# Optimization experiments

Measured on AMD Instinct MI355X. Metric: run time of the kernel, lower is better.

Reference implementation:

```python
import jax, jax.numpy as jnp
import numpy as np

B, N = 8, 2048
CLIP, D, BD, NC = 512, 256, 128, 10  # CLIP_EMBED_DIM, GNN_NODE_DIM, BOTTLENECK_DIM_GNN, NUM_CLASSES
LN_EPS = 1e-5


def _layer_norm(x, g, b):
    mu = jnp.mean(x, axis=-1, keepdims=True)
    var = jnp.mean(jnp.square(x - mu), axis=-1, keepdims=True)
    return (x - mu) / jnp.sqrt(var + LN_EPS) * g + b


def setup_inputs() -> dict:
    key = jax.random.key(0)
    ks = jax.random.split(key, 16)
    def w(k, shape, fan_in):
        lim = 1.0 / np.sqrt(fan_in)
        return jax.random.uniform(k, shape, jnp.float32, -lim, lim)
    return {
        "local_feat": jax.random.normal(ks[0], (B, N, CLIP), jnp.float32),
        "coords": jax.random.uniform(ks[1], (B, N, 2), jnp.float32),
        "mask": jax.random.randint(ks[2], (B, N), 0, 2).astype(bool),
        # node_encoder: Linear(CLIP->D) + LayerNorm(D)
        "enc_w": w(ks[3], (CLIP, D), CLIP), "enc_b": jnp.zeros((D,), jnp.float32),
        "enc_g": jnp.ones((D,), jnp.float32), "enc_beta": jnp.zeros((D,), jnp.float32),
        "gamma": jnp.asarray(5.0, jnp.float32),  # spatial_gamma
        "wq": w(ks[4], (D, D), D), "bq": jnp.zeros((D,), jnp.float32),
        "wk": w(ks[5], (D, D), D), "bk": jnp.zeros((D,), jnp.float32),
        "wv": w(ks[6], (D, D), D), "bv": jnp.zeros((D,), jnp.float32),
        # bottleneck: Linear(D->BD) + LayerNorm(BD)
        "bn_w": w(ks[7], (D, BD), D), "bn_b": jnp.zeros((BD,), jnp.float32),
        "bn_g": jnp.ones((BD,), jnp.float32), "bn_beta": jnp.zeros((BD,), jnp.float32),
        # classifier: Linear(BD->BD//2) + ReLU + Linear(BD//2->NC)
        "c1_w": w(ks[8], (BD, BD // 2), BD), "c1_b": jnp.zeros((BD // 2,), jnp.float32),
        "c2_w": w(ks[9], (BD // 2, NC), BD // 2), "c2_b": jnp.zeros((NC,), jnp.float32),
    }


def reference(local_feat, coords, mask, enc_w, enc_b, enc_g, enc_beta, gamma,
              wq, bq, wk, bk, wv, bv, bn_w, bn_b, bn_g, bn_beta,
              c1_w, c1_b, c2_w, c2_b):
    # node encoder: Linear + LN + ReLU -> h [B,N,D]
    h = jax.nn.relu(_layer_norm(local_feat @ enc_w + enc_b, enc_g, enc_beta))
    # pairwise euclidean distances on 2D coords (torch.cdist, under no_grad)
    xy = coords[:, :, :2]
    sq = jnp.sum(xy * xy, axis=-1)                                   # [B,N]
    d2 = sq[:, :, None] + sq[:, None, :] - 2.0 * jnp.einsum('bnd,bmd->bnm', xy, xy)
    dist = jax.lax.stop_gradient(jnp.sqrt(jnp.maximum(d2, 0.0)))     # [B,N,N]
    spatial_adj = jnp.exp(-dist * jnp.abs(gamma))
    q, k, v = h @ wq + bq, h @ wk + bk, h @ wv + bv
    scores = jnp.einsum('bnd,bmd->bnm', q, k) / jnp.sqrt(jnp.float32(D))
    attn = jax.nn.softmax(scores, axis=-1) * spatial_adj             # gated attention
    attn = jnp.where(mask[:, None, :], 0.0, attn)                    # zero masked keys
    agg = jnp.einsum('bnm,bmd->bnd', attn, v)                        # [B,N,D]
    out = jax.nn.relu(_layer_norm(agg @ bn_w + bn_b, bn_g, bn_beta)) # [B,N,BD]
    mask_v = (~mask)[:, :, None].astype(out.dtype)                   # [B,N,1]
    pooled = (out * mask_v).sum(axis=1) / jnp.maximum(mask_v.sum(axis=1), 1e-9)
    logits = jax.nn.relu(pooled @ c1_w + c1_b) @ c2_w + c2_b
    return logits, pooled
```

## Files before the change

kernel.cpp:

```cpp
#include <hip/hip_runtime.h>
#include <hip/hip_bf16.h>

typedef unsigned short ushort_t;
typedef __attribute__((ext_vector_type(8))) short s8;
typedef __attribute__((ext_vector_type(4))) float f4;
typedef __attribute__((ext_vector_type(16))) float f16v;

__device__ __forceinline__ unsigned short f2bf(float f) {
  union { float f; unsigned int u; } c; c.f = f;
  unsigned int r = (c.u + 0x7fffu + ((c.u >> 16) & 1u)) >> 16;
  return (unsigned short)r;
}
__device__ __forceinline__ float bf2f(ushort_t u) {
  union { unsigned int i; float f; } c; c.i = ((unsigned int)u) << 16; return c.f;
}
__device__ __forceinline__ uint4 pack8(float4 a, float4 b) {
  uint4 r;
  r.x = (unsigned)f2bf(a.x) | ((unsigned)f2bf(a.y) << 16);
  r.y = (unsigned)f2bf(a.z) | ((unsigned)f2bf(a.w) << 16);
  r.z = (unsigned)f2bf(b.x) | ((unsigned)f2bf(b.y) << 16);
  r.w = (unsigned)f2bf(b.z) | ((unsigned)f2bf(b.w) << 16);
  return r;
}
__device__ __forceinline__ void dma16(const ushort_t* g, const short* l) {
  __builtin_amdgcn_global_load_lds(
      (const __attribute__((address_space(1))) unsigned int*)g,
      (__attribute__((address_space(3))) unsigned int*)(unsigned long)l,
      16, 0, 0);
}

__global__ __launch_bounds__(256) void k_wt_all(
    const float* __restrict__ enc_w, const float* __restrict__ wq,
    const float* __restrict__ wk, const float* __restrict__ wv,
    const float* __restrict__ bn_w,
    ushort_t* __restrict__ enc_wT, ushort_t* __restrict__ wqkvT,
    ushort_t* __restrict__ bn_wT) {
  const int y = blockIdx.y;
  const int i = blockIdx.x * 256 + threadIdx.x;
  if (y == 0) {
    if (i < 131072) { const int n = i >> 9, k = i & 511; enc_wT[i] = f2bf(enc_w[k * 256 + n]); }
  } else if (y <= 3) {
    if (i < 65536) {
      const int n = i >> 8, k = i & 255;
      const float* src = (y == 1) ? wq : (y == 2) ? wk : wv;
      wqkvT[(y - 1) * 65536 + i] = f2bf(src[k * 256 + n]);
    }
  } else {
    if (i < 32768) { const int n = i >> 8, k = i & 255; bn_wT[i] = f2bf(bn_w[k * 128 + n]); }
  }
}

__global__ __launch_bounds__(256, 3) void k_gemm_enc(
    const float* __restrict__ A, const ushort_t* __restrict__ WT,
    const float* __restrict__ bia, const float* __restrict__ g,
    const float* __restrict__ beta, ushort_t* __restrict__ out) {
  __shared__ short Al[32 * 72];
  __shared__ short Bl[256 * 72];
  __shared__ float red1[32][2], red2[32][2];
  const int t = threadIdx.x;
  const int wv = t >> 6, lane = t & 63, l16 = lane & 15, quad = lane >> 4;
  const int wm = wv >> 1, wn = wv & 1;
  const int row0 = blockIdx.x * 32;

  f4 acc[8];
#pragma unroll
  for (int nf = 0; nf < 8; ++nf) acc[nf] = (f4){0.f, 0.f, 0.f, 0.f};

  for (int k0 = 0; k0 < 512; k0 += 64) {
    __syncthreads();
    {
      const int r = t >> 3, c8 = t & 7;
      const float* src = &A[(size_t)(row0 + r) * 512 + k0 + c8 * 8];
      *(uint4*)&Al[r * 72 + c8 * 8] =
          pack8(*(const float4*)src, *(const float4*)(src + 4));
    }
#pragma unroll
    for (int i = 0; i < 8; ++i) {
      const int ch = t + i * 256;
      const int r = ch >> 3, c8 = ch & 7;
      *(uint4*)&Bl[r * 72 + c8 * 8] =
          *(const uint4*)&WT[(size_t)r * 512 + k0 + c8 * 8];
    }
    __syncthreads();
#pragma unroll
    for (int kc = 0; kc < 2; ++kc) {
      const s8 af = *(const s8*)&Al[(wm * 16 + l16) * 72 + kc * 32 + quad * 8];
#pragma unroll
      for (int nf = 0; nf < 8; ++nf) {
        const s8 bf = *(const s8*)&Bl[(wn * 128 + nf * 16 + l16) * 72 + kc * 32 + quad * 8];
        acc[nf] = __builtin_amdgcn_mfma_f32_16x16x32_bf16(af, bf, acc[nf], 0, 0, 0);
      }
    }
  }
  float bi[8], gg[8], bb[8];
#pragma unroll
  for (int nf = 0; nf < 8; ++nf) {
    const int col = wn * 128 + nf * 16 + l16;
    bi[nf] = bia[col]; gg[nf] = g[col]; bb[nf] = beta[col];
  }
  float s1[4] = {0.f, 0.f, 0.f, 0.f}, s2[4] = {0.f, 0.f, 0.f, 0.f};
#pragma unroll
  for (int nf = 0; nf < 8; ++nf)
#pragma unroll
    for (int r = 0; r < 4; ++r) {
      const float v = acc[nf][r] + bi[nf];
      acc[nf][r] = v;
      s1[r] += v; s2[r] += v * v;
    }
#pragma unroll
  for (int m = 1; m < 16; m <<= 1) {
#pragma unroll
    for (int r = 0; r < 4; ++r) {
      s1[r] += __shfl_xor(s1[r], m);
      s2[r] += __shfl_xor(s2[r], m);
    }
  }
  if (l16 == 0) {
#pragma unroll
    for (int r = 0; r < 4; ++r) {
      const int rl = wm * 16 + quad * 4 + r;
      red1[rl][wn] = s1[r]; red2[rl][wn] = s2[r];
    }
  }
  __syncthreads();
#pragma unroll
  for (int r = 0; r < 4; ++r) {
    const int rl = wm * 16 + quad * 4 + r;
    const float mu = (red1[rl][0] + red1[rl][1]) * (1.f / 256.f);
    const float var = (red2[rl][0] + red2[rl][1]) * (1.f / 256.f) - mu * mu;
    const float rstd = rsqrtf(var + 1e-5f);
#pragma unroll
    for (int nf = 0; nf < 8; ++nf) {
      const int col = wn * 128 + nf * 16 + l16;
      const float v = (acc[nf][r] - mu) * rstd * gg[nf] + bb[nf];
      out[(size_t)(row0 + rl) * 256 + col] = f2bf(fmaxf(v, 0.f));
    }
  }
}

__global__ __launch_bounds__(256, 4) void k_gemm_qkv(
    const ushort_t* __restrict__ A, const ushort_t* __restrict__ WT,
    const float* __restrict__ bq, const float* __restrict__ bk,
    const float* __restrict__ bv,
    ushort_t* __restrict__ q, ushort_t* __restrict__ k, ushort_t* __restrict__ vt) {
  __shared__ short Al[64 * 72];
  __shared__ short Bl[128 * 72];
  const int t = threadIdx.x;
  const int wv = t >> 6, lane = t & 63, l16 = lane & 15, quad = lane >> 4;
  const int wm = wv >> 1, wn = wv & 1;
  const int row0 = blockIdx.x * 64;
  const int nb = blockIdx.y;
  const int type = nb >> 1;
  const ushort_t* wtb = WT + (size_t)nb * 128 * 256;

  f4 acc[2][4];
#pragma unroll
  for (int mf = 0; mf < 2; ++mf)
#pragma unroll
    for (int nf = 0; nf < 4; ++nf) acc[mf][nf] = (f4){0.f, 0.f, 0.f, 0.f};

  for (int k0 = 0; k0 < 256; k0 += 64) {
    __syncthreads();
#pragma unroll
    for (int i = 0; i < 2; ++i) {
      const int ch = t + i * 256;
      const int r = ch >> 3, c8 = ch & 7;
      *(uint4*)&Al[r * 72 + c8 * 8] =
          *(const uint4*)&A[(size_t)(row0 + r) * 256 + k0 + c8 * 8];
    }
#pragma unroll
    for (int i = 0; i < 4; ++i) {
      const int ch = t + i * 256;
      const int r = ch >> 3, c8 = ch & 7;
      *(uint4*)&Bl[r * 72 + c8 * 8] =
          *(const uint4*)&wtb[(size_t)r * 256 + k0 + c8 * 8];
    }
    __syncthreads();
#pragma unroll
    for (int kc = 0; kc < 2; ++kc) {
      s8 af[2];
      af[0] = *(const s8*)&Al[(wm * 32 + l16) * 72 + kc * 32 + quad * 8];
      af[1] = *(const s8*)&Al[(wm * 32 + 16 + l16) * 72 + kc * 32 + quad * 8];
#pragma unroll
      for (int nf = 0; nf < 4; ++nf) {
        const s8 bf = *(const s8*)&Bl[(wn * 64 + nf * 16 + l16) * 72 + kc * 32 + quad * 8];
        acc[0][nf] = __builtin_amdgcn_mfma_f32_16x16x32_bf16(af[0], bf, acc[0][nf], 0, 0, 0);
        acc[1][nf] = __builtin_amdgcn_mfma_f32_16x16x32_bf16(af[1], bf, acc[1][nf], 0, 0, 0);
      }
    }
  }
  const float* bias = (type == 0) ? bq : (type == 1) ? bk : bv;
#pragma unroll
  for (int nf = 0; nf < 4; ++nf) {
    const int colg = nb * 128 + wn * 64 + nf * 16 + l16;
    const int col = colg - type * 256;
    const float bi = bias[col];
    if (type == 2) {
      const int b = row0 >> 11;
#pragma unroll
      for (int mf = 0; mf < 2; ++mf) {
        const int n = (row0 & 2047) + wm * 32 + mf * 16 + quad * 4;
        ushort4 pk;
        pk.x = f2bf(acc[mf][nf][0] + bi);
        pk.y = f2bf(acc[mf][nf][1] + bi);
        pk.z = f2bf(acc[mf][nf][2] + bi);
        pk.w = f2bf(acc[mf][nf][3] + bi);
        *(ushort4*)&vt[((size_t)b * 256 + col) * 2048 + n] = pk;
      }
    } else {
      ushort_t* dst = (type == 0) ? q : k;
      const float sc = (type == 0) ? 0.0625f : 1.f;
#pragma unroll
      for (int mf = 0; mf < 2; ++mf)
#pragma unroll
        for (int r = 0; r < 4; ++r) {
          const int row = row0 + wm * 32 + mf * 16 + quad * 4 + r;
          dst[(size_t)row * 256 + col] = f2bf((acc[mf][nf][r] + bi) * sc);
        }
    }
  }
}

__global__ __launch_bounds__(256, 2) void k_attn(
    const ushort_t* __restrict__ qb, const ushort_t* __restrict__ kb,
    const ushort_t* __restrict__ vtb,
    const float* __restrict__ coords, const int* __restrict__ mask,
    const float* __restrict__ gam,
    ushort_t* __restrict__ Opb, float* __restrict__ lws) {
  __shared__ short kld[2][8192];
  __shared__ short vld[2][8192];
  __shared__ short pl[128 * 40];
  const int t = threadIdx.x;
  const int wv = t >> 6, lane = t & 63, l16 = lane & 15, quad = lane >> 4;
  const int hw = lane >> 5, l32 = lane & 31;
  const int b = blockIdx.z, ks = blockIdx.y;
  const int qw = blockIdx.x * 128 + wv * 32;
  const int kbase = ks * 512;

  float rcx[2][4], rcy[2][4];
#pragma unroll
  for (int mf = 0; mf < 2; ++mf)
#pragma unroll
    for (int r = 0; r < 4; ++r) {
      const float2 cc = ((const float2*)coords)[b * 2048 + qw + mf * 16 + quad * 4 + r];
      rcx[mf][r] = cc.x; rcy[mf][r] = cc.y;
    }
  const float gamma = fabsf(gam[0]);

  f16v o32[8];
#pragma unroll
  for (int i = 0; i < 8; ++i)
#pragma unroll
    for (int j = 0; j < 16; ++j) o32[i][j] = 0.f;
  float lrun[2][4];
#pragma unroll
  for (int mf = 0; mf < 2; ++mf)
#pragma unroll
    for (int r = 0; r < 4; ++r) lrun[mf][r] = 0.f;

  const ushort_t* kbb = kb + ((size_t)b * 2048 + kbase) * 256;
  const ushort_t* vbb = vtb + (size_t)b * 256 * 2048 + kbase;
  const ushort_t* qrow0 = qb + ((size_t)b * 2048 + qw + l16) * 256 + quad * 8;
  const ushort_t* qrow1 = qrow0 + 16 * 256;

#pragma unroll
  for (int i = 0; i < 4; ++i) {
    const int i2 = wv * 4 + i;
    dma16(kbb + (size_t)l32 * 256 + (i2 * 2 + hw) * 8, &kld[0][i2 * 512]);
    dma16(vbb + (size_t)(i * 64 + lane) * 2048 + wv * 8, &vld[0][(wv * 256 + i * 64) * 8]);
  }
  __syncthreads();

  for (int kt = 0; kt < 16; ++kt) {
    const int cur = kt & 1;
    const int m0 = kbase + kt * 32;
    if (kt < 15) {
      const ushort_t* kn = kbb + (size_t)(kt + 1) * 32 * 256;
      const ushort_t* vn = vbb + (kt + 1) * 32;
      const int nb2 = cur ^ 1;
#pragma unroll
      for (int i = 0; i < 4; ++i) {
        const int i2 = wv * 4 + i;
        dma16(kn + (size_t)l32 * 256 + (i2 * 2 + hw) * 8, &kld[nb2][i2 * 512]);
        dma16(vn + (size_t)(i * 64 + lane) * 2048 + wv * 8, &vld[nb2][(wv * 256 + i * 64) * 8]);
      }
    }
    f4 sc[2][2];
#pragma unroll
    for (int mf = 0; mf < 2; ++mf)
#pragma unroll
      for (int s = 0; s < 2; ++s) sc[mf][s] = (f4){0.f, 0.f, 0.f, 0.f};
#pragma unroll
    for (int c = 0; c < 8; ++c) {
      const s8 qa0 = *(const s8*)(qrow0 + c * 32);
      const s8 qa1 = *(const s8*)(qrow1 + c * 32);
#pragma unroll
      for (int s = 0; s < 2; ++s) {
        const s8 bfr = *(const s8*)&kld[cur][((c * 4 + quad) * 32 + s * 16 + l16) * 8];
        sc[0][s] = __builtin_amdgcn_mfma_f32_16x16x32_bf16(qa0, bfr, sc[0][s], 0, 0, 0);
        sc[1][s] = __builtin_amdgcn_mfma_f32_16x16x32_bf16(qa1, bfr, sc[1][s], 0, 0, 0);
      }
    }
#pragma unroll
    for (int s = 0; s < 2; ++s) {
      const int m = m0 + s * 16 + l16;
      const float2 cc = ((const float2*)coords)[b * 2048 + m];
      const float mfv = mask[b * 2048 + m] ? 0.f : 1.f;
#pragma unroll
      for (int mf = 0; mf < 2; ++mf)
#pragma unroll
        for (int r = 0; r < 4; ++r) {
          const float p = __expf(sc[mf][s][r]);
          lrun[mf][r] += p;
          const float dx = rcx[mf][r] - cc.x, dy = rcy[mf][r] - cc.y;
          const float dist = sqrtf(fmaxf(dx * dx + dy * dy, 0.f));
          const float w = p * __expf(-gamma * dist) * mfv;
          pl[(wv * 32 + mf * 16 + quad * 4 + r) * 40 + s * 16 + l16] = (short)f2bf(w);
        }
    }
    const s8 pa0 = *(const s8*)&pl[(wv * 32 + l32) * 40 + hw * 8];
    const s8 pa1 = *(const s8*)&pl[(wv * 32 + l32) * 40 + 16 + hw * 8];
#pragma unroll
    for (int dt = 0; dt < 8; ++dt) {
      const s8 bv0 = *(const s8*)&vld[cur][(hw * 256 + dt * 32 + l32) * 8];
      o32[dt] = __builtin_amdgcn_mfma_f32_32x32x16_bf16(pa0, bv0, o32[dt], 0, 0, 0);
      const s8 bv1 = *(const s8*)&vld[cur][((2 + hw) * 256 + dt * 32 + l32) * 8];
      o32[dt] = __builtin_amdgcn_mfma_f32_32x32x16_bf16(pa1, bv1, o32[dt], 0, 0, 0);
    }
    __syncthreads();
  }
  ushort_t* OpK = Opb + (size_t)ks * 4194304;
#pragma unroll
  for (int dt = 0; dt < 8; ++dt) {
#pragma unroll
    for (int reg = 0; reg < 16; ++reg) {
      const int row = (reg & 3) + 8 * (reg >> 2) + 4 * hw;
      OpK[((size_t)b * 2048 + qw + row) * 256 + dt * 32 + l32] = f2bf(o32[dt][reg]);
    }
  }
#pragma unroll
  for (int o2 = 1; o2 < 16; o2 <<= 1) {
#pragma unroll
    for (int mf = 0; mf < 2; ++mf)
#pragma unroll
      for (int r = 0; r < 4; ++r) lrun[mf][r] += __shfl_xor(lrun[mf][r], o2);
  }
  if (l16 == 0) {
#pragma unroll
    for (int mf = 0; mf < 2; ++mf)
#pragma unroll
      for (int r = 0; r < 4; ++r)
        lws[ks * 16384 + b * 2048 + qw + mf * 16 + quad * 4 + r] = lrun[mf][r];
  }
}

__global__ __launch_bounds__(256, 3) void k_gemm_bn(
    const ushort_t* __restrict__ Opb, const float* __restrict__ lws,
    const ushort_t* __restrict__ WT,
    const float* __restrict__ bia, const float* __restrict__ g,
    const float* __restrict__ beta, ushort_t* __restrict__ out) {
  __shared__ short Al[32 * 72];
  __shared__ short Bl[128 * 72];
  __shared__ float red1[32][2], red2[32][2];
  __shared__ float sCm[32];
  const int t = threadIdx.x;
  const int wv = t >> 6, lane = t & 63, l16 = lane & 15, quad = lane >> 4;
  const int wm = wv >> 1, wn = wv & 1;
  const int row0 = blockIdx.x * 32;

  if (t < 32) {
    const int row = row0 + t;
    sCm[t] = 1.f / (lws[row] + lws[16384 + row] + lws[32768 + row] + lws[49152 + row]);
  }

  f4 acc[4];
#pragma unroll
  for (int nf = 0; nf < 4; ++nf) acc[nf] = (f4){0.f, 0.f, 0.f, 0.f};

  for (int k0 = 0; k0 < 256; k0 += 64) {
    __syncthreads();
    {
      const int r = t >> 3, c8 = t & 7;
      const float c0 = sCm[r];
      const size_t off = (size_t)(row0 + r) * 256 + k0 + c8 * 8;
      float e[8];
#pragma unroll
      for (int j = 0; j < 8; ++j) e[j] = 0.f;
#pragma unroll
      for (int pp = 0; pp < 4; ++pp) {
        const uint4 u = *(const uint4*)&Opb[(size_t)pp * 4194304 + off];
        e[0] += bf2f((ushort_t)(u.x & 0xffff)); e[1] += bf2f((ushort_t)(u.x >> 16));
        e[2] += bf2f((ushort_t)(u.y & 0xffff)); e[3] += bf2f((ushort_t)(u.y >> 16));
        e[4] += bf2f((ushort_t)(u.z & 0xffff)); e[5] += bf2f((ushort_t)(u.z >> 16));
        e[6] += bf2f((ushort_t)(u.w & 0xffff)); e[7] += bf2f((ushort_t)(u.w >> 16));
      }
      float4 ea = {c0 * e[0], c0 * e[1], c0 * e[2], c0 * e[3]};
      float4 eb = {c0 * e[4], c0 * e[5], c0 * e[6], c0 * e[7]};
      *(uint4*)&Al[r * 72 + c8 * 8] = pack8(ea, eb);
    }
#pragma unroll
    for (int i = 0; i < 4; ++i) {
      const int ch = t + i * 256;
      const int r = ch >> 3, c8 = ch & 7;
      *(uint4*)&Bl[r * 72 + c8 * 8] =
          *(const uint4*)&WT[(size_t)r * 256 + k0 + c8 * 8];
    }
    __syncthreads();
#pragma unroll
    for (int kc = 0; kc < 2; ++kc) {
      const s8 af = *(const s8*)&Al[(wm * 16 + l16) * 72 + kc * 32 + quad * 8];
#pragma unroll
      for (int nf = 0; nf < 4; ++nf) {
        const s8 bf = *(const s8*)&Bl[(wn * 64 + nf * 16 + l16) * 72 + kc * 32 + quad * 8];
        acc[nf] = __builtin_amdgcn_mfma_f32_16x16x32_bf16(af, bf, acc[nf], 0, 0, 0);
      }
    }
  }
  float bi[4], gg[4], bb[4];
#pragma unroll
  for (int nf = 0; nf < 4; ++nf) {
    const int col = wn * 64 + nf * 16 + l16;
    bi[nf] = bia[col]; gg[nf] = g[col]; bb[nf] = beta[col];
  }
  float s1[4] = {0.f, 0.f, 0.f, 0.f}, s2[4] = {0.f, 0.f, 0.f, 0.f};
#pragma unroll
  for (int nf = 0; nf < 4; ++nf)
#pragma unroll
    for (int r = 0; r < 4; ++r) {
      const float v = acc[nf][r] + bi[nf];
      acc[nf][r] = v;
      s1[r] += v; s2[r] += v * v;
    }
#pragma unroll
  for (int m = 1; m < 16; m <<= 1) {
#pragma unroll
    for (int r = 0; r < 4; ++r) {
      s1[r] += __shfl_xor(s1[r], m);
      s2[r] += __shfl_xor(s2[r], m);
    }
  }
  if (l16 == 0) {
#pragma unroll
    for (int r = 0; r < 4; ++r) {
      const int rl = wm * 16 + quad * 4 + r;
      red1[rl][wn] = s1[r]; red2[rl][wn] = s2[r];
    }
  }
  __syncthreads();
#pragma unroll
  for (int r = 0; r < 4; ++r) {
    const int rl = wm * 16 + quad * 4 + r;
    const float mu = (red1[rl][0] + red1[rl][1]) * (1.f / 128.f);
    const float var = (red2[rl][0] + red2[rl][1]) * (1.f / 128.f) - mu * mu;
    const float rstd = rsqrtf(var + 1e-5f);
#pragma unroll
    for (int nf = 0; nf < 4; ++nf) {
      const int col = wn * 64 + nf * 16 + l16;
      const float v = (acc[nf][r] - mu) * rstd * gg[nf] + bb[nf];
      out[(size_t)(row0 + rl) * 128 + col] = f2bf(fmaxf(v, 0.f));
    }
  }
}

__global__ __launch_bounds__(128) void k_pool1(
    const ushort_t* __restrict__ obn, const int* __restrict__ mask,
    float* __restrict__ pp) {
  const int g = blockIdx.x, b = blockIdx.y, d = threadIdx.x;
  const ushort_t* ob = obn + ((size_t)b * 2048 + g * 128) * 128;
  const int* mb = mask + b * 2048 + g * 128;
  float s = 0.f, cnt = 0.f;
  for (int n = 0; n < 128; ++n) {
    const float w = mb[n] ? 0.f : 1.f;
    s += w * bf2f(ob[(size_t)n * 128 + d]);
    cnt += w;
  }
  pp[(b * 16 + g) * 132 + d] = s;
  if (d == 0) pp[(b * 16 + g) * 132 + 128] = cnt;
}

__global__ __launch_bounds__(128) void k_pool2_head(
    const float* __restrict__ pp, const float* __restrict__ c1w,
    const float* __restrict__ c1b, const float* __restrict__ c2w,
    const float* __restrict__ c2b, float* __restrict__ dout) {
  __shared__ float ps[128];
  __shared__ float h1[64];
  const int b = blockIdx.x, t = threadIdx.x;
  float s = 0.f, cnt = 0.f;
  for (int g = 0; g < 16; ++g) {
    s += pp[(b * 16 + g) * 132 + t];
    cnt += pp[(b * 16 + g) * 132 + 128];
  }
  const float p = s / fmaxf(cnt, 1e-9f);
  ps[t] = p;
  dout[80 + b * 128 + t] = p;
  __syncthreads();
  if (t < 64) {
    float acc = c1b[t];
    for (int d = 0; d < 128; ++d) acc += ps[d] * c1w[d * 64 + t];
    h1[t] = fmaxf(acc, 0.f);
  }
  __syncthreads();
  if (t < 10) {
    float a2 = c2b[t];
    for (int j = 0; j < 64; ++j) a2 += h1[j] * c2w[j * 10 + t];
    dout[b * 10 + t] = a2;
  }
}

extern "C" void kernel_launch(void* const* d_in, const int* in_sizes, int n_in,
                              void* d_out, int out_size, void* d_ws, size_t ws_size,
                              hipStream_t stream) {
  const float* lf     = (const float*)d_in[0];
  const float* coords = (const float*)d_in[1];
  const int*   mask   = (const int*)d_in[2];
  const float* enc_w  = (const float*)d_in[3];
  const float* enc_b  = (const float*)d_in[4];
  const float* enc_g  = (const float*)d_in[5];
  const float* enc_be = (const float*)d_in[6];
  const float* gamma  = (const float*)d_in[7];
  const float* wq     = (const float*)d_in[8];
  const float* bq     = (const float*)d_in[9];
  const float* wk     = (const float*)d_in[10];
  const float* bk     = (const float*)d_in[11];
  const float* wv     = (const float*)d_in[12];
  const float* bv     = (const float*)d_in[13];
  const float* bn_w   = (const float*)d_in[14];
  const float* bn_b   = (const float*)d_in[15];
  const float* bn_g   = (const float*)d_in[16];
  const float* bn_be  = (const float*)d_in[17];
  const float* c1w    = (const float*)d_in[18];
  const float* c1b    = (const float*)d_in[19];
  const float* c2w    = (const float*)d_in[20];
  const float* c2b    = (const float*)d_in[21];

  float* ws = (float*)d_ws;
  ushort_t* h_bf   = (ushort_t*)ws;
  ushort_t* q_bf   = (ushort_t*)(ws + 2097152);
  ushort_t* k_bf   = (ushort_t*)(ws + 4194304);
  ushort_t* vt_bf  = (ushort_t*)(ws + 6291456);
  ushort_t* Opb    = (ushort_t*)(ws + 8388608);
  ushort_t* obn_bf = (ushort_t*)(ws + 16777216);
  ushort_t* enc_wT = (ushort_t*)(ws + 17825792);
  ushort_t* wqkvT  = (ushort_t*)(ws + 17891328);
  ushort_t* bn_wT  = (ushort_t*)(ws + 17989632);
  float*    lws    = ws + 18006016;
  float*    ppart  = ws + 18071552;
  float* out = (float*)d_out;

  k_wt_all<<<dim3(512, 5), 256, 0, stream>>>(enc_w, wq, wk, wv, bn_w,
                                             enc_wT, wqkvT, bn_wT);
  k_gemm_enc<<<512, 256, 0, stream>>>(lf, enc_wT, enc_b, enc_g, enc_be, h_bf);
  k_gemm_qkv<<<dim3(256, 6), 256, 0, stream>>>(h_bf, wqkvT, bq, bk, bv, q_bf, k_bf, vt_bf);
  k_attn<<<dim3(16, 4, 8), 256, 0, stream>>>(q_bf, k_bf, vt_bf, coords, mask, gamma,
                                             Opb, lws);
  k_gemm_bn<<<512, 256, 0, stream>>>(Opb, lws, bn_wT, bn_b, bn_g, bn_be, obn_bf);
  k_pool1<<<dim3(16, 8), 128, 0, stream>>>(obn_bf, mask, ppart);
  k_pool2_head<<<8, 128, 0, stream>>>(ppart, c1w, c1b, c2w, c2b, out);
}
```

Before: 259.7 us.

## Shrink attention tiles to 16 queries per wave with 16x16 MFMA for P·V

Restructures the attention kernel so each wave handles 16 query rows instead of 32, with 16-key tiles instead of 32. The P·V product switches from 32x32x16 to 16x16x32 MFMA, and the upper half of the P tile is zero-padded. The grid doubles and launch bounds rise to 3 blocks per CU, which cuts registers and LDS per block to raise occupancy. In exchange, each K/V tile is reused by fewer queries, so total K/V loads double. Half of each P·V MFMA multiplies padding zeros, and there are twice as many loop iterations with a barrier each.

```diff
diff --git a/kernel.cpp b/kernel.cpp
--- a/kernel.cpp
+++ b/kernel.cpp
@@ -4,7 +4,6 @@
 typedef unsigned short ushort_t;
 typedef __attribute__((ext_vector_type(8))) short s8;
 typedef __attribute__((ext_vector_type(4))) float f4;
-typedef __attribute__((ext_vector_type(16))) float f16v;
 
 __device__ __forceinline__ unsigned short f2bf(float f) {
   union { float f; unsigned int u; } c; c.f = f;
@@ -221,136 +220,114 @@
   }
 }
 
-__global__ __launch_bounds__(256, 2) void k_attn(
+__global__ __launch_bounds__(256, 3) void k_attn(
     const ushort_t* __restrict__ qb, const ushort_t* __restrict__ kb,
     const ushort_t* __restrict__ vtb,
     const float* __restrict__ coords, const int* __restrict__ mask,
     const float* __restrict__ gam,
     ushort_t* __restrict__ Opb, float* __restrict__ lws) {
-  __shared__ short kld[2][8192];
-  __shared__ short vld[2][8192];
-  __shared__ short pl[128 * 40];
+  __shared__ short kld[2][4096];
+  __shared__ short vld[2][4096];
+  __shared__ short pl[64 * 40];
   const int t = threadIdx.x;
   const int wv = t >> 6, lane = t & 63, l16 = lane & 15, quad = lane >> 4;
-  const int hw = lane >> 5, l32 = lane & 31;
   const int b = blockIdx.z, ks = blockIdx.y;
-  const int qw = blockIdx.x * 128 + wv * 32;
+  const int qw = blockIdx.x * 64 + wv * 16;
   const int kbase = ks * 512;
 
-  float rcx[2][4], rcy[2][4];
-#pragma unroll
-  for (int mf = 0; mf < 2; ++mf)
-#pragma unroll
-    for (int r = 0; r < 4; ++r) {
-      const float2 cc = ((const float2*)coords)[b * 2048 + qw + mf * 16 + quad * 4 + r];
-      rcx[mf][r] = cc.x; rcy[mf][r] = cc.y;
-    }
+  {
+    unsigned int* z = (unsigned int*)&pl[(t >> 2) * 40 + 16 + (t & 3) * 4];
+    z[0] = 0u; z[1] = 0u;
+  }
+
+  float rcx[4], rcy[4];
+#pragma unroll
+  for (int r = 0; r < 4; ++r) {
+    const float2 cc = ((const float2*)coords)[b * 2048 + qw + quad * 4 + r];
+    rcx[r] = cc.x; rcy[r] = cc.y;
+  }
   const float gamma = fabsf(gam[0]);
 
-  f16v o32[8];
-#pragma unroll
-  for (int i = 0; i < 8; ++i)
-#pragma unroll
-    for (int j = 0; j < 16; ++j) o32[i][j] = 0.f;
-  float lrun[2][4];
-#pragma unroll
-  for (int mf = 0; mf < 2; ++mf)
-#pragma unroll
-    for (int r = 0; r < 4; ++r) lrun[mf][r] = 0.f;
+  f4 o16[16];
+#pragma unroll
+  for (int i = 0; i < 16; ++i) o16[i] = (f4){0.f, 0.f, 0.f, 0.f};
+  float lrun[4] = {0.f, 0.f, 0.f, 0.f};
 
   const ushort_t* kbb = kb + ((size_t)b * 2048 + kbase) * 256;
   const ushort_t* vbb = vtb + (size_t)b * 256 * 2048 + kbase;
-  const ushort_t* qrow0 = qb + ((size_t)b * 2048 + qw + l16) * 256 + quad * 8;
-  const ushort_t* qrow1 = qrow0 + 16 * 256;
-
-#pragma unroll
-  for (int i = 0; i < 4; ++i) {
-    const int i2 = wv * 4 + i;
-    dma16(kbb + (size_t)l32 * 256 + (i2 * 2 + hw) * 8, &kld[0][i2 * 512]);
-    dma16(vbb + (size_t)(i * 64 + lane) * 2048 + wv * 8, &vld[0][(wv * 256 + i * 64) * 8]);
+  const ushort_t* qrow = qb + ((size_t)b * 2048 + qw + l16) * 256 + quad * 8;
+
+#pragma unroll
+  for (int i = 0; i < 2; ++i) {
+    const int i2 = wv * 2 + i;
+    dma16(kbb + (size_t)(lane & 15) * 256 + (i2 * 4 + (lane >> 4)) * 8,
+          &kld[0][i2 * 512]);
+    dma16(vbb + (size_t)(i2 * 32 + (lane >> 1)) * 2048 + (lane & 1) * 8,
+          &vld[0][i2 * 512]);
   }
   __syncthreads();
 
-  for (int kt = 0; kt < 16; ++kt) {
+  for (int kt = 0; kt < 32; ++kt) {
     const int cur = kt & 1;
-    const int m0 = kbase + kt * 32;
-    if (kt < 15) {
-      const ushort_t* kn = kbb + (size_t)(kt + 1) * 32 * 256;
-      const ushort_t* vn = vbb + (kt + 1) * 32;
+    const int m0 = kbase + kt * 16;
+    if (kt < 31) {
+      const ushort_t* kn = kbb + (size_t)(kt + 1) * 16 * 256;
+      const ushort_t* vn = vbb + (kt + 1) * 16;
       const int nb2 = cur ^ 1;
 #pragma unroll
-      for (int i = 0; i < 4; ++i) {
-        const int i2 = wv * 4 + i;
-        dma16(kn + (size_t)l32 * 256 + (i2 * 2 + hw) * 8, &kld[nb2][i2 * 512]);
-        dma16(vn + (size_t)(i * 64 + lane) * 2048 + wv * 8, &vld[nb2][(wv * 256 + i * 64) * 8]);
-      }
-    }
-    f4 sc[2][2];
-#pragma unroll
-    for (int mf = 0; mf < 2; ++mf)
-#pragma unroll
-      for (int s = 0; s < 2; ++s) sc[mf][s] = (f4){0.f, 0.f, 0.f, 0.f};
+      for (int i = 0; i < 2; ++i) {
+        const int i2 = wv * 2 + i;
+        dma16(kn + (size_t)(lane & 15) * 256 + (i2 * 4 + (lane >> 4)) * 8,
+              &kld[nb2][i2 * 512]);
+        dma16(vn + (size_t)(i2 * 32 + (lane >> 1)) * 2048 + (lane & 1) * 8,
+              &vld[nb2][i2 * 512]);
+      }
+    }
+    f4 sc = (f4){0.f, 0.f, 0.f, 0.f};
 #pragma unroll
     for (int c = 0; c < 8; ++c) {
-      const s8 qa0 = *(const s8*)(qrow0 + c * 32);
-      const s8 qa1 = *(const s8*)(qrow1 + c * 32);
-#pragma unroll
-      for (int s = 0; s < 2; ++s) {
-        const s8 bfr = *(const s8*)&kld[cur][((c * 4 + quad) * 32 + s * 16 + l16) * 8];
-        sc[0][s] = __builtin_amdgcn_mfma_f32_16x16x32_bf16(qa0, bfr, sc[0][s], 0, 0, 0);
-        sc[1][s] = __builtin_amdgcn_mfma_f32_16x16x32_bf16(qa1, bfr, sc[1][s], 0, 0, 0);
-      }
-    }
-#pragma unroll
-    for (int s = 0; s < 2; ++s) {
-      const int m = m0 + s * 16 + l16;
+      const s8 qa = *(const s8*)(qrow + c * 32);
+      const s8 bfr = *(const s8*)&kld[cur][((c * 4 + quad) * 16 + l16) * 8];
+      sc = __builtin_amdgcn_mfma_f32_16x16x32_bf16(qa, bfr, sc, 0, 0, 0);
+    }
+    {
+      const int m = m0 + l16;
       const float2 cc = ((const float2*)coords)[b * 2048 + m];
       const float mfv = mask[b * 2048 + m] ? 0.f : 1.f;
 #pragma unroll
-      for (int mf = 0; mf < 2; ++mf)
-#pragma unroll
-        for (int r = 0; r < 4; ++r) {
-          const float p = __expf(sc[mf][s][r]);
-          lrun[mf][r] += p;
-          const float dx = rcx[mf][r] - cc.x, dy = rcy[mf][r] - cc.y;
-          const float dist = sqrtf(fmaxf(dx * dx + dy * dy, 0.f));
-          const float w = p * __expf(-gamma * dist) * mfv;
-          pl[(wv * 32 + mf * 16 + quad * 4 + r) * 40 + s * 16 + l16] = (short)f2bf(w);
-        }
-    }
-    const s8 pa0 = *(const s8*)&pl[(wv * 32 + l32) * 40 + hw * 8];
-    const s8 pa1 = *(const s8*)&pl[(wv * 32 + l32) * 40 + 16 + hw * 8];
-#pragma unroll
-    for (int dt = 0; dt < 8; ++dt) {
-      const s8 bv0 = *(const s8*)&vld[cur][(hw * 256 + dt * 32 + l32) * 8];
-      o32[dt] = __builtin_amdgcn_mfma_f32_32x32x16_bf16(pa0, bv0, o32[dt], 0, 0, 0);
-      const s8 bv1 = *(const s8*)&vld[cur][((2 + hw) * 256 + dt * 32 + l32) * 8];
-      o32[dt] = __builtin_amdgcn_mfma_f32_32x32x16_bf16(pa1, bv1, o32[dt], 0, 0, 0);
+      for (int r = 0; r < 4; ++r) {
+        const float p = __expf(sc[r]);
+        lrun[r] += p;
+        const float dx = rcx[r] - cc.x, dy = rcy[r] - cc.y;
+        const float dist = sqrtf(fmaxf(dx * dx + dy * dy, 0.f));
+        const float w = p * __expf(-gamma * dist) * mfv;
+        pl[(wv * 16 + quad * 4 + r) * 40 + l16] = (short)f2bf(w);
+      }
+    }
+    const s8 pa = *(const s8*)&pl[(wv * 16 + l16) * 40 + quad * 8];
+#pragma unroll
+    for (int df = 0; df < 16; ++df) {
+      const s8 bv = *(const s8*)&vld[cur][((df * 16 + l16) * 16) + (quad & 1) * 8];
+      o16[df] = __builtin_amdgcn_mfma_f32_16x16x32_bf16(pa, bv, o16[df], 0, 0, 0);
     }
     __syncthreads();
   }
   ushort_t* OpK = Opb + (size_t)ks * 4194304;
 #pragma unroll
-  for (int dt = 0; dt < 8; ++dt) {
-#pragma unroll
-    for (int reg = 0; reg < 16; ++reg) {
-      const int row = (reg & 3) + 8 * (reg >> 2) + 4 * hw;
-      OpK[((size_t)b * 2048 + qw + row) * 256 + dt * 32 + l32] = f2bf(o32[dt][reg]);
-    }
+  for (int r = 0; r < 4; ++r) {
+    ushort_t* orow = OpK + ((size_t)b * 2048 + qw + quad * 4 + r) * 256 + l16;
+#pragma unroll
+    for (int df = 0; df < 16; ++df) orow[df * 16] = f2bf(o16[df][r]);
   }
 #pragma unroll
   for (int o2 = 1; o2 < 16; o2 <<= 1) {
 #pragma unroll
-    for (int mf = 0; mf < 2; ++mf)
-#pragma unroll
-      for (int r = 0; r < 4; ++r) lrun[mf][r] += __shfl_xor(lrun[mf][r], o2);
+    for (int r = 0; r < 4; ++r) lrun[r] += __shfl_xor(lrun[r], o2);
   }
   if (l16 == 0) {
 #pragma unroll
-    for (int mf = 0; mf < 2; ++mf)
-#pragma unroll
-      for (int r = 0; r < 4; ++r)
-        lws[ks * 16384 + b * 2048 + qw + mf * 16 + quad * 4 + r] = lrun[mf][r];
+    for (int r = 0; r < 4; ++r)
+      lws[ks * 16384 + b * 2048 + qw + quad * 4 + r] = lrun[r];
   }
 }
 
@@ -551,7 +528,7 @@
                                              enc_wT, wqkvT, bn_wT);
   k_gemm_enc<<<512, 256, 0, stream>>>(lf, enc_wT, enc_b, enc_g, enc_be, h_bf);
   k_gemm_qkv<<<dim3(256, 6), 256, 0, stream>>>(h_bf, wqkvT, bq, bk, bv, q_bf, k_bf, vt_bf);
-  k_attn<<<dim3(16, 4, 8), 256, 0, stream>>>(q_bf, k_bf, vt_bf, coords, mask, gamma,
+  k_attn<<<dim3(32, 4, 8), 256, 0, stream>>>(q_bf, k_bf, vt_bf, coords, mask, gamma,
                                              Opb, lws);
   k_gemm_bn<<<512, 256, 0, stream>>>(Opb, lws, bn_wT, bn_b, bn_g, bn_be, obn_bf);
   k_pool1<<<dim3(16, 8), 128, 0, stream>>>(obn_bf, mask, ppart);
```

Result: slower. 301.8 us (+16.2%).

## Fuse masked mean pooling into bottleneck GEMM epilogue via atomics

Applied to the files above, without the earlier changes.

The bottleneck GEMM epilogue now multiplies each LayerNorm+ReLU output row by a precomputed mask weight, reduces across the wave with shuffles, and atomically adds into a per-batch pooled accumulator. This removes the bf16 intermediate write and re-read and the separate pool1 kernel. A small kernel zeroes the accumulator and precomputes mask weights, and the head kernel recomputes the unmasked count. The trade is contended float atomics and nondeterministic summation order, plus leftover dummy declarations.

```diff
diff --git a/kernel.cpp b/kernel.cpp
--- a/kernel.cpp
+++ b/kernel.cpp
@@ -358,7 +358,7 @@
     const ushort_t* __restrict__ Opb, const float* __restrict__ lws,
     const ushort_t* __restrict__ WT,
     const float* __restrict__ bia, const float* __restrict__ g,
-    const float* __restrict__ beta, ushort_t* __restrict__ out) {
+    const float* __restrict__ beta, float* __restrict__ pooledAcc) {
   __shared__ short Al[32 * 72];
   __shared__ short Bl[128 * 72];
   __shared__ float red1[32][2], red2[32][2];
@@ -367,6 +367,7 @@
   const int wv = t >> 6, lane = t & 63, l16 = lane & 15, quad = lane >> 4;
   const int wm = wv >> 1, wn = wv & 1;
   const int row0 = blockIdx.x * 32;
+  const int b = row0 >> 11;
 
   if (t < 32) {
     const int row = row0 + t;
@@ -447,50 +448,71 @@
     }
   }
   __syncthreads();
+  float colsum[4] = {0.f, 0.f, 0.f, 0.f};
+  const int* mrow = (const int*)0;
 #pragma unroll
   for (int r = 0; r < 4; ++r) {
     const int rl = wm * 16 + quad * 4 + r;
     const float mu = (red1[rl][0] + red1[rl][1]) * (1.f / 128.f);
     const float var = (red2[rl][0] + red2[rl][1]) * (1.f / 128.f) - mu * mu;
     const float rstd = rsqrtf(var + 1e-5f);
+    extern const int* __mask_dummy;
 #pragma unroll
     for (int nf = 0; nf < 4; ++nf) {
-      const int col = wn * 64 + nf * 16 + l16;
       const float v = (acc[nf][r] - mu) * rstd * gg[nf] + bb[nf];
-      out[(size_t)(row0 + rl) * 128 + col] = f2bf(fmaxf(v, 0.f));
-    }
-  }
-}
-
-__global__ __launch_bounds__(128) void k_pool1(
-    const ushort_t* __restrict__ obn, const int* __restrict__ mask,
-    float* __restrict__ pp) {
-  const int g = blockIdx.x, b = blockIdx.y, d = threadIdx.x;
-  const ushort_t* ob = obn + ((size_t)b * 2048 + g * 128) * 128;
-  const int* mb = mask + b * 2048 + g * 128;
-  float s = 0.f, cnt = 0.f;
-  for (int n = 0; n < 128; ++n) {
-    const float w = mb[n] ? 0.f : 1.f;
-    s += w * bf2f(ob[(size_t)n * 128 + d]);
-    cnt += w;
-  }
-  pp[(b * 16 + g) * 132 + d] = s;
-  if (d == 0) pp[(b * 16 + g) * 132 + 128] = cnt;
+      acc[nf][r] = fmaxf(v, 0.f);
+    }
+  }
+  (void)mrow;
+  {
+    float mw[4];
+#pragma unroll
+    for (int r = 0; r < 4; ++r) {
+      const int rl = wm * 16 + quad * 4 + r;
+      mw[r] = pooledAcc[1024 + row0 + rl] ;
+    }
+#pragma unroll
+    for (int nf = 0; nf < 4; ++nf) {
+      float s = acc[nf][0] * mw[0] + acc[nf][1] * mw[1] +
+                acc[nf][2] * mw[2] + acc[nf][3] * mw[3];
+      s += __shfl_xor(s, 16);
+      s += __shfl_xor(s, 32);
+      if (quad == 0) {
+        const int col = wn * 64 + nf * 16 + l16;
+        atomicAdd(&pooledAcc[b * 128 + col], s);
+      }
+    }
+  }
+}
+
+__global__ __launch_bounds__(256) void k_maskf(const int* __restrict__ mask,
+                                               float* __restrict__ pooledAcc) {
+  const int i = blockIdx.x * 256 + threadIdx.x;
+  if (i < 16384) pooledAcc[1024 + i] = mask[i] ? 0.f : 1.f;
+  if (i < 1024) pooledAcc[i] = 0.f;
 }
 
 __global__ __launch_bounds__(128) void k_pool2_head(
-    const float* __restrict__ pp, const float* __restrict__ c1w,
-    const float* __restrict__ c1b, const float* __restrict__ c2w,
-    const float* __restrict__ c2b, float* __restrict__ dout) {
+    const float* __restrict__ pooledAcc, const int* __restrict__ mask,
+    const float* __restrict__ c1w, const float* __restrict__ c1b,
+    const float* __restrict__ c2w, const float* __restrict__ c2b,
+    float* __restrict__ dout) {
   __shared__ float ps[128];
   __shared__ float h1[64];
+  __shared__ float scnt[128];
   const int b = blockIdx.x, t = threadIdx.x;
-  float s = 0.f, cnt = 0.f;
-  for (int g = 0; g < 16; ++g) {
-    s += pp[(b * 16 + g) * 132 + t];
-    cnt += pp[(b * 16 + g) * 132 + 128];
-  }
-  const float p = s / fmaxf(cnt, 1e-9f);
+  float c = 0.f;
+  const int* mb = mask + b * 2048 + t * 16;
+#pragma unroll
+  for (int j = 0; j < 16; ++j) c += mb[j] ? 0.f : 1.f;
+  scnt[t] = c;
+  __syncthreads();
+  for (int o2 = 64; o2 > 0; o2 >>= 1) {
+    if (t < o2) scnt[t] += scnt[t + o2];
+    __syncthreads();
+  }
+  const float cnt = scnt[0];
+  const float p = pooledAcc[b * 128 + t] / fmaxf(cnt, 1e-9f);
   ps[t] = p;
   dout[80 + b * 128 + t] = p;
   __syncthreads();
@@ -539,21 +561,20 @@
   ushort_t* k_bf   = (ushort_t*)(ws + 4194304);
   ushort_t* vt_bf  = (ushort_t*)(ws + 6291456);
   ushort_t* Opb    = (ushort_t*)(ws + 8388608);
-  ushort_t* obn_bf = (ushort_t*)(ws + 16777216);
   ushort_t* enc_wT = (ushort_t*)(ws + 17825792);
   ushort_t* wqkvT  = (ushort_t*)(ws + 17891328);
   ushort_t* bn_wT  = (ushort_t*)(ws + 17989632);
   float*    lws    = ws + 18006016;
-  float*    ppart  = ws + 18071552;
+  float*    pooledAcc = ws + 18071552;
   float* out = (float*)d_out;
 
   k_wt_all<<<dim3(512, 5), 256, 0, stream>>>(enc_w, wq, wk, wv, bn_w,
                                              enc_wT, wqkvT, bn_wT);
+  k_maskf<<<64, 256, 0, stream>>>(mask, pooledAcc);
   k_gemm_enc<<<512, 256, 0, stream>>>(lf, enc_wT, enc_b, enc_g, enc_be, h_bf);
   k_gemm_qkv<<<dim3(256, 6), 256, 0, stream>>>(h_bf, wqkvT, bq, bk, bv, q_bf, k_bf, vt_bf);
   k_attn<<<dim3(16, 4, 8), 256, 0, stream>>>(q_bf, k_bf, vt_bf, coords, mask, gamma,
                                              Opb, lws);
-  k_gemm_bn<<<512, 256, 0, stream>>>(Opb, lws, bn_wT, bn_b, bn_g, bn_be, obn_bf);
-  k_pool1<<<dim3(16, 8), 128, 0, stream>>>(obn_bf, mask, ppart);
-  k_pool2_head<<<8, 128, 0, stream>>>(ppart, c1w, c1b, c2w, c2b, out);
-}
+  k_gemm_bn<<<512, 256, 0, stream>>>(Opb, lws, bn_wT, bn_b, bn_g, bn_be, pooledAcc);
+  k_pool2_head<<<8, 128, 0, stream>>>(pooledAcc, mask, c1w, c1b, c2w, c2b, out);
+}
```

Result: no change. 258.7 us (-0.4%).
